# Optimization experiments

Measured on AMD Instinct MI355X. Metric: run time of the kernel, lower is better.

Reference implementation:

```python
import jax, jax.numpy as jnp
import numpy as np

B, N, D = 2, 2048, 1024
H = 16
HD = D // H  # 64
ROPE_BASE = 10000.0


def setup_inputs() -> dict:
    key = jax.random.key(0)
    ks = jax.random.split(key, 5)
    s = 0.02
    return {
        "x": jax.random.normal(ks[0], (B, N, D), dtype=jnp.float32),
        "qkv_w": jax.random.normal(ks[1], (3 * D, D), dtype=jnp.float32) * s,
        "qkv_b": jax.random.normal(ks[2], (3 * D,), dtype=jnp.float32) * s,
        "proj_w": jax.random.normal(ks[3], (D, D), dtype=jnp.float32) * s,
        "proj_b": jax.random.normal(ks[4], (D,), dtype=jnp.float32) * s,
    }


def _rotate_half(t):
    # interleaved pairs: (x1,x2) -> (-x2,x1), matching lucidrains RotaryEmbedding
    t = t.reshape(*t.shape[:-1], -1, 2)
    x1, x2 = t[..., 0], t[..., 1]
    return jnp.stack((-x2, x1), axis=-1).reshape(*t.shape[:-2], -1)


def _apply_rope(t, cos, sin):
    # t: [B, H, N, HD]; cos/sin: [N, HD]
    return t * cos + _rotate_half(t) * sin


def reference(x, qkv_w, qkv_b, proj_w, proj_b):
    b, n, d = x.shape
    scale = HD ** -0.5

    qkv = x @ qkv_w.T + qkv_b                      # [B, N, 3D]
    qkv = qkv.reshape(b, n, 3, H, HD)
    qkv = jnp.transpose(qkv, (2, 0, 3, 1, 4))       # [3, B, H, N, HD]
    q, k, v = qkv[0], qkv[1], qkv[2]

    # RoPE (lang freqs, interpolate_factor=1)
    inv_freq = 1.0 / (ROPE_BASE ** (jnp.arange(0, HD, 2, dtype=jnp.float32) / HD))
    freqs = jnp.arange(n, dtype=jnp.float32)[:, None] * inv_freq[None, :]  # [N, HD/2]
    freqs = jnp.repeat(freqs, 2, axis=-1)           # [N, HD] interleaved
    cos, sin = jnp.cos(freqs), jnp.sin(freqs)
    q = _apply_rope(q, cos, sin)
    k = _apply_rope(k, cos, sin)

    scores = jnp.einsum('bhid,bhjd->bhij', q, k) * scale  # [B, H, N, N]
    causal = jnp.triu(jnp.ones((n, n), dtype=bool), k=1)
    scores = jnp.where(causal, -jnp.inf, scores)
    attn = jax.nn.softmax(scores, axis=-1)

    out = jnp.einsum('bhij,bhjd->bhid', attn, v)    # [B, H, N, HD]
    out = jnp.transpose(out, (0, 2, 1, 3)).reshape(b, n, d)
    return out @ proj_w.T + proj_b
```

## Files before the change

### kernel.cpp

```cpp
#include <hip/hip_runtime.h>
#include <hip/hip_bf16.h>
#include <cstdint>
#include <cstddef>

typedef __hip_bfloat16 bf16;
typedef short bf16x8 __attribute__((ext_vector_type(8)));
typedef float f32x4 __attribute__((ext_vector_type(4)));
typedef int i32x4 __attribute__((ext_vector_type(4)));

#define MFMA16(a, b, c) __builtin_amdgcn_mfma_f32_16x16x32_bf16((a), (b), (c), 0, 0, 0)

__global__ void cvt_f32_bf16(const float* __restrict__ in, bf16* __restrict__ out, int n4)
{
    int i = blockIdx.x * blockDim.x + threadIdx.x;
    if (i >= n4) return;
    float4 v = *reinterpret_cast<const float4*>(in + (size_t)i * 4);
    __align__(8) bf16 tmp[4];
    tmp[0] = __float2bfloat16(v.x);
    tmp[1] = __float2bfloat16(v.y);
    tmp[2] = __float2bfloat16(v.z);
    tmp[3] = __float2bfloat16(v.w);
    *reinterpret_cast<short4*>(out + (size_t)i * 4) = *reinterpret_cast<short4*>(tmp);
}

__global__ void rope_table_kernel(float2* __restrict__ tab)
{
    int i = blockIdx.x * blockDim.x + threadIdx.x;
    int pos = i >> 5, f = i & 31;
    float inv = powf(10000.f, -(float)f * (1.f / 32.f));
    float ang = (float)pos * inv;
    tab[i] = make_float2(cosf(ang), sinf(ang));
}

__global__ void rope_apply_kernel(bf16* __restrict__ qkv, const float2* __restrict__ tab)
{
    int idx = blockIdx.x * blockDim.x + threadIdx.x;
    int row = idx >> 8;
    int cc  = (idx & 255) * 8;
    int pos = row & 2047;
    int hd  = cc & 63;
    bf16* p = qkv + (size_t)row * 3072 + cc;
    i32x4 v = *reinterpret_cast<const i32x4*>(p);
    bf16* e = reinterpret_cast<bf16*>(&v);
    const float2* tb = tab + pos * 32 + (hd >> 1);
#pragma unroll
    for (int pp = 0; pp < 4; ++pp) {
        float2 cs = tb[pp];
        float x1 = __bfloat162float(e[2 * pp]);
        float x2 = __bfloat162float(e[2 * pp + 1]);
        e[2 * pp]     = __float2bfloat16(x1 * cs.x - x2 * cs.y);
        e[2 * pp + 1] = __float2bfloat16(x2 * cs.x + x1 * cs.y);
    }
    *reinterpret_cast<i32x4*>(p) = v;
}

__device__ inline void store_out(float* p, float v) { *p = v; }
__device__ inline void store_out(bf16* p, float v) { *p = __float2bfloat16(v); }

template <typename OutT>
__global__ void gemm_bt_kernel(const bf16* __restrict__ A, const bf16* __restrict__ BT,
                               const float* __restrict__ bias, OutT* __restrict__ C,
                               int M, int N, int K)
{
    constexpr int BM = 128, BN = 128, BK = 32, LDT = BK + 8;
    __shared__ __align__(16) bf16 Al[BM * LDT];
    __shared__ __align__(16) bf16 Bl[BN * LDT];

    const int tid = threadIdx.x;
    const int l = tid & 63;
    const int w = tid >> 6;
    const int wr = w >> 1, wc = w & 1;
    const int lane15 = l & 15, lhi = l >> 4;
    const int row0 = blockIdx.x * BM, col0 = blockIdx.y * BN;

    const int c0 = tid, c1 = tid + 256;
    const bf16* Ag0 = A + (size_t)(row0 + (c0 >> 2)) * K + (c0 & 3) * 8;
    const bf16* Ag1 = A + (size_t)(row0 + (c1 >> 2)) * K + (c1 & 3) * 8;
    const bf16* Bg0 = BT + (size_t)(col0 + (c0 >> 2)) * K + (c0 & 3) * 8;
    const bf16* Bg1 = BT + (size_t)(col0 + (c1 >> 2)) * K + (c1 & 3) * 8;
    bf16* sA0 = &Al[(c0 >> 2) * LDT + (c0 & 3) * 8];
    bf16* sA1 = &Al[(c1 >> 2) * LDT + (c1 & 3) * 8];
    bf16* sB0 = &Bl[(c0 >> 2) * LDT + (c0 & 3) * 8];
    bf16* sB1 = &Bl[(c1 >> 2) * LDT + (c1 & 3) * 8];

    f32x4 acc[4][4] = {};

    i32x4 ra0 = *reinterpret_cast<const i32x4*>(Ag0);
    i32x4 ra1 = *reinterpret_cast<const i32x4*>(Ag1);
    i32x4 rb0 = *reinterpret_cast<const i32x4*>(Bg0);
    i32x4 rb1 = *reinterpret_cast<const i32x4*>(Bg1);

    for (int k0 = 0; k0 < K; k0 += BK) {
        __syncthreads();
        *reinterpret_cast<i32x4*>(sA0) = ra0;
        *reinterpret_cast<i32x4*>(sA1) = ra1;
        *reinterpret_cast<i32x4*>(sB0) = rb0;
        *reinterpret_cast<i32x4*>(sB1) = rb1;
        __syncthreads();
        if (k0 + BK < K) {
            ra0 = *reinterpret_cast<const i32x4*>(Ag0 + k0 + BK);
            ra1 = *reinterpret_cast<const i32x4*>(Ag1 + k0 + BK);
            rb0 = *reinterpret_cast<const i32x4*>(Bg0 + k0 + BK);
            rb1 = *reinterpret_cast<const i32x4*>(Bg1 + k0 + BK);
        }
        bf16x8 af[4], bfr[4];
#pragma unroll
        for (int m = 0; m < 4; ++m)
            af[m] = *reinterpret_cast<const bf16x8*>(&Al[(wr * 64 + m * 16 + lane15) * LDT + lhi * 8]);
#pragma unroll
        for (int n = 0; n < 4; ++n)
            bfr[n] = *reinterpret_cast<const bf16x8*>(&Bl[(wc * 64 + n * 16 + lane15) * LDT + lhi * 8]);
#pragma unroll
        for (int m = 0; m < 4; ++m)
#pragma unroll
            for (int n = 0; n < 4; ++n)
                acc[m][n] = MFMA16(af[m], bfr[n], acc[m][n]);
    }

#pragma unroll
    for (int m = 0; m < 4; ++m) {
#pragma unroll
        for (int n = 0; n < 4; ++n) {
            int col = col0 + wc * 64 + n * 16 + lane15;
            float bs = bias[col];
#pragma unroll
            for (int j = 0; j < 4; ++j) {
                int row = row0 + wr * 64 + m * 16 + lhi * 4 + j;
                store_out(&C[(size_t)row * N + col], acc[m][n][j] + bs);
            }
        }
    }
}

__global__ void attn_kernel(const bf16* __restrict__ qkv, bf16* __restrict__ outp)
{
    constexpr int LDK = 72;
    __shared__ __align__(16) bf16 Kl[64 * LDK];
    __shared__ __align__(16) bf16 Vt[64 * LDK];
    __shared__ __align__(16) bf16 Pl[64 * LDK];

    const int bh = blockIdx.x;
    const int b = bh >> 4, h = bh & 15;
    const int q0 = blockIdx.y * 64;
    const int tid = threadIdx.x;
    const int w = tid >> 6, l = tid & 63;
    const int lane15 = l & 15, lhi = l >> 4;

    const size_t RS = 3072;
    const bf16* base = qkv + (size_t)b * 2048 * RS;

    bf16x8 qf0, qf1;
    {
        const bf16* qr = base + (size_t)(q0 + w * 16 + lane15) * RS + h * 64 + lhi * 8;
        qf0 = *reinterpret_cast<const bf16x8*>(qr);
        qf1 = *reinterpret_cast<const bf16x8*>(qr + 32);
    }

    float m_run[4], l_run[4];
    f32x4 o_acc[4] = {};
#pragma unroll
    for (int j = 0; j < 4; ++j) { m_run[j] = -1e30f; l_run[j] = 0.f; }

    const int ntiles = q0 / 64 + 1;
    for (int t = 0; t < ntiles; ++t) {
        const int kv0 = t * 64;
        __syncthreads();
#pragma unroll
        for (int cc = 0; cc < 2; ++cc) {
            int c = tid + cc * 256;
            int r = c >> 3, c8 = (c & 7) * 8;
            i32x4 v = *reinterpret_cast<const i32x4*>(base + (size_t)(kv0 + r) * RS + 1024 + h * 64 + c8);
            *reinterpret_cast<i32x4*>(&Kl[r * LDK + c8]) = v;
        }
#pragma unroll
        for (int cc = 0; cc < 2; ++cc) {
            int c = tid + cc * 256;
            int r = c >> 3, c8 = (c & 7) * 8;
            i32x4 v = *reinterpret_cast<const i32x4*>(base + (size_t)(kv0 + r) * RS + 2048 + h * 64 + c8);
            const bf16* pv = reinterpret_cast<const bf16*>(&v);
#pragma unroll
            for (int i = 0; i < 8; ++i) Vt[(c8 + i) * LDK + r] = pv[i];
        }
        __syncthreads();

        f32x4 s[4] = {};
#pragma unroll
        for (int n = 0; n < 4; ++n) {
            bf16x8 kf0 = *reinterpret_cast<const bf16x8*>(&Kl[(n * 16 + lane15) * LDK + lhi * 8]);
            bf16x8 kf1 = *reinterpret_cast<const bf16x8*>(&Kl[(n * 16 + lane15) * LDK + 32 + lhi * 8]);
            s[n] = MFMA16(qf0, kf0, s[n]);
            s[n] = MFMA16(qf1, kf1, s[n]);
        }

        const int qrow = q0 + w * 16 + lhi * 4;
#pragma unroll
        for (int n = 0; n < 4; ++n) {
            const int kvc = kv0 + n * 16 + lane15;
#pragma unroll
            for (int j = 0; j < 4; ++j) {
                float v = s[n][j] * 0.125f;
                s[n][j] = (kvc > qrow + j) ? -1e30f : v;
            }
        }

        float alpha[4];
#pragma unroll
        for (int j = 0; j < 4; ++j) {
            float rm = fmaxf(fmaxf(s[0][j], s[1][j]), fmaxf(s[2][j], s[3][j]));
            rm = fmaxf(rm, __shfl_xor(rm, 1));
            rm = fmaxf(rm, __shfl_xor(rm, 2));
            rm = fmaxf(rm, __shfl_xor(rm, 4));
            rm = fmaxf(rm, __shfl_xor(rm, 8));
            float mnew = fmaxf(m_run[j], rm);
            alpha[j] = __expf(m_run[j] - mnew);
            m_run[j] = mnew;
        }
        float rs[4] = {0.f, 0.f, 0.f, 0.f};
#pragma unroll
        for (int n = 0; n < 4; ++n)
#pragma unroll
            for (int j = 0; j < 4; ++j) {
                float p = __expf(s[n][j] - m_run[j]);
                s[n][j] = p;
                rs[j] += p;
            }
#pragma unroll
        for (int j = 0; j < 4; ++j) {
            float r = rs[j];
            r += __shfl_xor(r, 1);
            r += __shfl_xor(r, 2);
            r += __shfl_xor(r, 4);
            r += __shfl_xor(r, 8);
            l_run[j] = l_run[j] * alpha[j] + r;
            o_acc[0][j] *= alpha[j];
            o_acc[1][j] *= alpha[j];
            o_acc[2][j] *= alpha[j];
            o_acc[3][j] *= alpha[j];
        }

        bf16* Pw = &Pl[w * 16 * LDK];
#pragma unroll
        for (int n = 0; n < 4; ++n)
#pragma unroll
            for (int j = 0; j < 4; ++j)
                Pw[(lhi * 4 + j) * LDK + n * 16 + lane15] = __float2bfloat16(s[n][j]);

        bf16x8 pa0 = *reinterpret_cast<const bf16x8*>(&Pw[lane15 * LDK + lhi * 8]);
        bf16x8 pa1 = *reinterpret_cast<const bf16x8*>(&Pw[lane15 * LDK + 32 + lhi * 8]);
#pragma unroll
        for (int t2 = 0; t2 < 4; ++t2) {
            bf16x8 vf0 = *reinterpret_cast<const bf16x8*>(&Vt[(t2 * 16 + lane15) * LDK + lhi * 8]);
            bf16x8 vf1 = *reinterpret_cast<const bf16x8*>(&Vt[(t2 * 16 + lane15) * LDK + 32 + lhi * 8]);
            o_acc[t2] = MFMA16(pa0, vf0, o_acc[t2]);
            o_acc[t2] = MFMA16(pa1, vf1, o_acc[t2]);
        }
    }

#pragma unroll
    for (int j = 0; j < 4; ++j) {
        float inv = 1.f / l_run[j];
        size_t row = (size_t)(b * 2048 + q0 + w * 16 + lhi * 4 + j);
#pragma unroll
        for (int t2 = 0; t2 < 4; ++t2)
            outp[row * 1024 + h * 64 + t2 * 16 + lane15] = __float2bfloat16(o_acc[t2][j] * inv);
    }
}

extern "C" void kernel_launch(void* const* d_in, const int* in_sizes, int n_in,
                              void* d_out, int out_size, void* d_ws, size_t ws_size,
                              hipStream_t stream)
{
    const float* x      = (const float*)d_in[0];
    const float* qkv_w  = (const float*)d_in[1];
    const float* qkv_b  = (const float*)d_in[2];
    const float* proj_w = (const float*)d_in[3];
    const float* proj_b = (const float*)d_in[4];
    float* out = (float*)d_out;

    char* ws = (char*)d_ws;
    bf16* x_bf   = (bf16*)ws;  ws += (size_t)4096 * 1024 * 2;
    bf16* wq_bf  = (bf16*)ws;  ws += (size_t)3072 * 1024 * 2;
    bf16* wp_bf  = (bf16*)ws;  ws += (size_t)1024 * 1024 * 2;
    bf16* qkvbuf = (bf16*)ws;  ws += (size_t)4096 * 3072 * 2;
    bf16* aout   = (bf16*)ws;  ws += (size_t)4096 * 1024 * 2;
    float2* tab  = (float2*)ws;

    cvt_f32_bf16<<<4096, 256, 0, stream>>>(x, x_bf, 1048576);
    cvt_f32_bf16<<<3072, 256, 0, stream>>>(qkv_w, wq_bf, 786432);
    cvt_f32_bf16<<<1024, 256, 0, stream>>>(proj_w, wp_bf, 262144);
    rope_table_kernel<<<256, 256, 0, stream>>>(tab);

    gemm_bt_kernel<bf16><<<dim3(32, 24), 256, 0, stream>>>(x_bf, wq_bf, qkv_b, qkvbuf, 4096, 3072, 1024);
    rope_apply_kernel<<<4096, 256, 0, stream>>>(qkvbuf, tab);
    attn_kernel<<<dim3(32, 32), 256, 0, stream>>>(qkvbuf, aout);
    gemm_bt_kernel<float><<<dim3(32, 8), 256, 0, stream>>>(aout, wp_bf, proj_b, out, 4096, 1024, 1024);
}
```

Measured before the change: 268.1 us.

## Use direct global-to-LDS loads in GEMM, reverse attention tile order, restructure V transpose

The GEMM now loads A/B tiles with global_load_lds straight into unpadded shared memory. This drops the register staging and the prefetch of the next tile, so the loop no longer overlaps the next load with compute, and the unpadded layout risks LDS bank conflicts. The attention kernel launches the longest causal query tiles first to balance the load, and builds the transposed V tile by having each lane gather 16 strided bf16 values and write two 16-byte chunks instead of 8 scalar LDS stores.

```diff
diff --git a/kernel.cpp b/kernel.cpp
--- a/kernel.cpp
+++ b/kernel.cpp
@@ -9,6 +9,13 @@
 typedef int i32x4 __attribute__((ext_vector_type(4)));
 
 #define MFMA16(a, b, c) __builtin_amdgcn_mfma_f32_16x16x32_bf16((a), (b), (c), 0, 0, 0)
+
+__device__ __forceinline__ void glds16(const bf16* g, bf16* l)
+{
+    __builtin_amdgcn_global_load_lds(
+        (const __attribute__((address_space(1))) void*)g,
+        (__attribute__((address_space(3))) void*)l, 16, 0, 0);
+}
 
 __global__ void cvt_f32_bf16(const float* __restrict__ in, bf16* __restrict__ out, int n4)
 {
@@ -62,54 +69,45 @@
                                const float* __restrict__ bias, OutT* __restrict__ C,
                                int M, int N, int K)
 {
-    constexpr int BM = 128, BN = 128, BK = 32, LDT = BK + 8;
-    __shared__ __align__(16) bf16 Al[BM * LDT];
-    __shared__ __align__(16) bf16 Bl[BN * LDT];
+    constexpr int BM = 128, BN = 128, BK = 32;
+    __shared__ __align__(16) bf16 Al[BM * BK];
+    __shared__ __align__(16) bf16 Bl[BN * BK];
 
     const int tid = threadIdx.x;
     const int l = tid & 63;
     const int w = tid >> 6;
     const int wr = w >> 1, wc = w & 1;
-    const int lane15 = l & 15, lhi = l >> 4;
+    const int l15 = l & 15, lhi = l >> 4;
     const int row0 = blockIdx.x * BM, col0 = blockIdx.y * BN;
 
-    const int c0 = tid, c1 = tid + 256;
-    const bf16* Ag0 = A + (size_t)(row0 + (c0 >> 2)) * K + (c0 & 3) * 8;
-    const bf16* Ag1 = A + (size_t)(row0 + (c1 >> 2)) * K + (c1 & 3) * 8;
-    const bf16* Bg0 = BT + (size_t)(col0 + (c0 >> 2)) * K + (c0 & 3) * 8;
-    const bf16* Bg1 = BT + (size_t)(col0 + (c1 >> 2)) * K + (c1 & 3) * 8;
-    bf16* sA0 = &Al[(c0 >> 2) * LDT + (c0 & 3) * 8];
-    bf16* sA1 = &Al[(c1 >> 2) * LDT + (c1 & 3) * 8];
-    bf16* sB0 = &Bl[(c0 >> 2) * LDT + (c0 & 3) * 8];
-    bf16* sB1 = &Bl[(c1 >> 2) * LDT + (c1 & 3) * 8];
+    const int ar0 = tid >> 2, ar1 = (tid + 256) >> 2;
+    const int ac  = (tid & 3) * 8;
+    const bf16* Ag0 = A + (size_t)(row0 + ar0) * K + ac;
+    const bf16* Ag1 = A + (size_t)(row0 + ar1) * K + ac;
+    const bf16* Bg0 = BT + (size_t)(col0 + ar0) * K + ac;
+    const bf16* Bg1 = BT + (size_t)(col0 + ar1) * K + ac;
+    const int wbase = (tid & 192) * 8;
+    bf16* sA0 = &Al[wbase];
+    bf16* sA1 = &Al[2048 + wbase];
+    bf16* sB0 = &Bl[wbase];
+    bf16* sB1 = &Bl[2048 + wbase];
 
     f32x4 acc[4][4] = {};
 
-    i32x4 ra0 = *reinterpret_cast<const i32x4*>(Ag0);
-    i32x4 ra1 = *reinterpret_cast<const i32x4*>(Ag1);
-    i32x4 rb0 = *reinterpret_cast<const i32x4*>(Bg0);
-    i32x4 rb1 = *reinterpret_cast<const i32x4*>(Bg1);
-
     for (int k0 = 0; k0 < K; k0 += BK) {
         __syncthreads();
-        *reinterpret_cast<i32x4*>(sA0) = ra0;
-        *reinterpret_cast<i32x4*>(sA1) = ra1;
-        *reinterpret_cast<i32x4*>(sB0) = rb0;
-        *reinterpret_cast<i32x4*>(sB1) = rb1;
-        __syncthreads();
-        if (k0 + BK < K) {
-            ra0 = *reinterpret_cast<const i32x4*>(Ag0 + k0 + BK);
-            ra1 = *reinterpret_cast<const i32x4*>(Ag1 + k0 + BK);
-            rb0 = *reinterpret_cast<const i32x4*>(Bg0 + k0 + BK);
-            rb1 = *reinterpret_cast<const i32x4*>(Bg1 + k0 + BK);
-        }
+        glds16(Ag0 + k0, sA0);
+        glds16(Ag1 + k0, sA1);
+        glds16(Bg0 + k0, sB0);
+        glds16(Bg1 + k0, sB1);
+        __syncthreads();
         bf16x8 af[4], bfr[4];
 #pragma unroll
         for (int m = 0; m < 4; ++m)
-            af[m] = *reinterpret_cast<const bf16x8*>(&Al[(wr * 64 + m * 16 + lane15) * LDT + lhi * 8]);
+            af[m] = *reinterpret_cast<const bf16x8*>(&Al[(wr * 64 + m * 16 + l15) * BK + lhi * 8]);
 #pragma unroll
         for (int n = 0; n < 4; ++n)
-            bfr[n] = *reinterpret_cast<const bf16x8*>(&Bl[(wc * 64 + n * 16 + lane15) * LDT + lhi * 8]);
+            bfr[n] = *reinterpret_cast<const bf16x8*>(&Bl[(wc * 64 + n * 16 + l15) * BK + lhi * 8]);
 #pragma unroll
         for (int m = 0; m < 4; ++m)
 #pragma unroll
@@ -121,7 +119,7 @@
     for (int m = 0; m < 4; ++m) {
 #pragma unroll
         for (int n = 0; n < 4; ++n) {
-            int col = col0 + wc * 64 + n * 16 + lane15;
+            int col = col0 + wc * 64 + n * 16 + l15;
             float bs = bias[col];
 #pragma unroll
             for (int j = 0; j < 4; ++j) {
@@ -141,7 +139,7 @@
 
     const int bh = blockIdx.x;
     const int b = bh >> 4, h = bh & 15;
-    const int q0 = blockIdx.y * 64;
+    const int q0 = (31 - blockIdx.y) * 64;
     const int tid = threadIdx.x;
     const int w = tid >> 6, l = tid & 63;
     const int lane15 = l & 15, lhi = l >> 4;
@@ -172,14 +170,15 @@
             i32x4 v = *reinterpret_cast<const i32x4*>(base + (size_t)(kv0 + r) * RS + 1024 + h * 64 + c8);
             *reinterpret_cast<i32x4*>(&Kl[r * LDK + c8]) = v;
         }
-#pragma unroll
-        for (int cc = 0; cc < 2; ++cc) {
-            int c = tid + cc * 256;
-            int r = c >> 3, c8 = (c & 7) * 8;
-            i32x4 v = *reinterpret_cast<const i32x4*>(base + (size_t)(kv0 + r) * RS + 2048 + h * 64 + c8);
-            const bf16* pv = reinterpret_cast<const bf16*>(&v);
-#pragma unroll
-            for (int i = 0; i < 8; ++i) Vt[(c8 + i) * LDK + r] = pv[i];
+        {
+            const int hd = l;
+            const int seg = w;
+            const bf16* vcol = base + (size_t)(kv0 + seg * 16) * RS + 2048 + h * 64 + hd;
+            __align__(16) bf16 tmp[16];
+#pragma unroll
+            for (int j = 0; j < 16; ++j) tmp[j] = vcol[(size_t)j * RS];
+            *reinterpret_cast<i32x4*>(&Vt[hd * LDK + seg * 16])     = *reinterpret_cast<const i32x4*>(&tmp[0]);
+            *reinterpret_cast<i32x4*>(&Vt[hd * LDK + seg * 16 + 8]) = *reinterpret_cast<const i32x4*>(&tmp[8]);
         }
         __syncthreads();
 
```

New measurement: 220.5 us. 17.7% less time.
